# Performance work log

Measured on AMD Instinct MI355X. Metric: run time of the kernel, lower is better.

The kernel has to match this reference:

```python
import jax, jax.numpy as jnp
import numpy as np

D_MODEL = 512
NUM_HEADS = 8
LN_EPS = 1e-5


def _linear(x, W, b):
    # torch nn.Linear: y = x @ W.T + b, W is [out, in]
    return x @ W.T + b


def _layernorm(x, g, b):
    mu = jnp.mean(x, axis=-1, keepdims=True)
    var = jnp.mean((x - mu) ** 2, axis=-1, keepdims=True)
    return (x - mu) * jax.lax.rsqrt(var + LN_EPS) * g + b


def _proj_block(x, W1, b1, ln_g, ln_b, W2, b2):
    # Linear -> LayerNorm -> GELU(exact) -> Linear
    h = _linear(x, W1, b1)
    h = _layernorm(h, ln_g, ln_b)
    h = jax.nn.gelu(h, approximate=False)
    return _linear(h, W2, b2)


def setup_inputs() -> dict:
    key = jax.random.key(0)
    ks = jax.random.split(key, 16)
    d = D_MODEL
    B, N = 32, 50000
    s = 0.02
    inp = {
        "query_features": jax.random.normal(ks[0], (B, d), jnp.float32),
        "candidate_features": jax.random.normal(ks[1], (N, d), jnp.float32),
        # temperature param init: log(1/0.07)
        "temperature": jnp.asarray(np.log(1.0 / 0.07), jnp.float32),
        # query projection
        "qW1": jax.random.normal(ks[2], (d, d), jnp.float32) * s,
        "qb1": jnp.zeros((d,), jnp.float32),
        "q_ln_g": jnp.ones((d,), jnp.float32),
        "q_ln_b": jnp.zeros((d,), jnp.float32),
        "qW2": jax.random.normal(ks[3], (d, d), jnp.float32) * s,
        "qb2": jnp.zeros((d,), jnp.float32),
        # key projection
        "kW1": jax.random.normal(ks[4], (d, d), jnp.float32) * s,
        "kb1": jnp.zeros((d,), jnp.float32),
        "k_ln_g": jnp.ones((d,), jnp.float32),
        "k_ln_b": jnp.zeros((d,), jnp.float32),
        "kW2": jax.random.normal(ks[5], (d, d), jnp.float32) * s,
        "kb2": jnp.zeros((d,), jnp.float32),
        # MultiheadAttention in-proj (only q/k needed for attn weights)
        "in_proj_w": jax.random.normal(ks[6], (3 * d, d), jnp.float32) * s,
        "in_proj_b": jnp.zeros((3 * d,), jnp.float32),
        # similarity fusion MLP: 3 -> 64 -> 1
        "fW1": jax.random.normal(ks[7], (64, 3), jnp.float32) * 0.5,
        "fb1": jnp.zeros((64,), jnp.float32),
        "fW2": jax.random.normal(ks[8], (1, 64), jnp.float32) * 0.5,
        "fb2": jnp.zeros((1,), jnp.float32),
    }
    return inp


def reference(query_features, candidate_features, temperature,
              qW1, qb1, q_ln_g, q_ln_b, qW2, qb2,
              kW1, kb1, k_ln_g, k_ln_b, kW2, kb2,
              in_proj_w, in_proj_b, fW1, fb1, fW2, fb2):
    d = D_MODEL
    H = NUM_HEADS
    dh = d // H

    qp = _proj_block(query_features, qW1, qb1, q_ln_g, q_ln_b, qW2, qb2)      # [B, d]
    kp = _proj_block(candidate_features, kW1, kb1, k_ln_g, k_ln_b, kW2, kb2)  # [N, d]

    # 1) cosine similarity with learnable temperature
    qn = qp / jnp.linalg.norm(qp, axis=-1, keepdims=True)
    kn = kp / jnp.linalg.norm(kp, axis=-1, keepdims=True)
    cosine_sim = (qn @ kn.T) * jnp.exp(temperature)                            # [B, N]

    # 2) euclidean similarity (||q-k|| via quadratic expansion, no [B,N,D] temp)
    q2 = jnp.sum(qp * qp, axis=-1)[:, None]
    k2 = jnp.sum(kp * kp, axis=-1)[None, :]
    d2 = jnp.maximum(q2 + k2 - 2.0 * (qp @ kp.T), 0.0)
    euclidean_sim = 1.0 / (1.0 + jnp.sqrt(d2))                                 # [B, N]

    # 3) attention-weight similarity (torch MHA weights, averaged over heads)
    Wq, Wk = in_proj_w[:d], in_proj_w[d:2 * d]
    bq, bk = in_proj_b[:d], in_proj_b[d:2 * d]
    q = (_linear(qp, Wq, bq)).reshape(-1, H, dh)                               # [B, H, dh]
    k = (_linear(kp, Wk, bk)).reshape(-1, H, dh)                               # [N, H, dh]
    scores = jnp.einsum('bhd,nhd->bhn', q, k) / jnp.sqrt(jnp.float32(dh))      # [B, H, N]
    attn_w = jax.nn.softmax(scores, axis=-1)
    learned_sim = jnp.mean(attn_w, axis=1)                                     # [B, N]

    # fusion MLP over stacked [B, N, 3]
    sims = jnp.stack([cosine_sim, euclidean_sim, learned_sim], axis=-1)
    h = jax.nn.relu(_linear(sims, fW1, fb1))                                   # [B, N, 64]
    out = jax.nn.sigmoid(_linear(h, fW2, fb2))[..., 0]                         # [B, N]
    return out
```

## Files before the change

### kernel.cpp

```cpp
#include <hip/hip_runtime.h>
#include <math.h>

#define D    512
#define BQ   32
#define NH   8
#define MT   64
#define NT   512

typedef _Float16 h2  __attribute__((ext_vector_type(2)));
typedef _Float16 h4v __attribute__((ext_vector_type(4)));
typedef _Float16 h8  __attribute__((ext_vector_type(8)));
typedef float    f4  __attribute__((ext_vector_type(4)));

typedef const __attribute__((address_space(1))) void gas_void;
typedef __attribute__((address_space(3))) void las_void;

__device__ __forceinline__ f4 MF(h8 a, h8 b, f4 c) {
  return __builtin_amdgcn_mfma_f32_16x16x32_f16(a, b, c, 0, 0, 0);
}

__device__ __forceinline__ float erf_fast(float x) {
    float ax = fabsf(x);
    float tt = 1.0f / fmaf(0.3275911f, ax, 1.0f);
    float poly = tt * fmaf(tt, fmaf(tt, fmaf(tt, fmaf(tt, 1.061405429f, -1.453152027f),
                          1.421413741f), -0.284496736f), 0.254829592f);
    float r = 1.0f - poly * __expf(-ax * ax);
    return copysignf(r, x);
}
__device__ __forceinline__ float gelu_fast(float x) {
    return 0.5f * x * (1.0f + erf_fast(x * 0.7071067811865475f));
}
__device__ __forceinline__ float gelu_exact(float x) {
    return 0.5f * x * (1.0f + erff(x * 0.7071067811865475f));
}

__global__ __launch_bounds__(256) void qproj_kernel(
    const float* __restrict__ xq,
    const float* __restrict__ W1, const float* __restrict__ b1,
    const float* __restrict__ lng, const float* __restrict__ lnb,
    const float* __restrict__ W2, const float* __restrict__ b2,
    const float* __restrict__ Wio, const float* __restrict__ bio,
    float* __restrict__ qp, float* __restrict__ qv,
    float* __restrict__ q2o, float* __restrict__ qinvo,
    _Float16* __restrict__ qph)
{
    __shared__ float xs[D];
    __shared__ float hs[D];
    __shared__ float red[16];
    const int t = threadIdx.x;
    const int row = blockIdx.x;

    for (int i = t; i < D; i += 256) xs[i] = xq[row * D + i];
    __syncthreads();

    float a0 = 0.f, a1 = 0.f;
    for (int i = 0; i < D; i += 4) {
        float4 xv = *(const float4*)&xs[i];
        float4 w0 = *(const float4*)&W1[(size_t)t * D + i];
        float4 w1 = *(const float4*)&W1[(size_t)(t + 256) * D + i];
        a0 += xv.x*w0.x + xv.y*w0.y + xv.z*w0.z + xv.w*w0.w;
        a1 += xv.x*w1.x + xv.y*w1.y + xv.z*w1.z + xv.w*w1.w;
    }
    float h0 = a0 + b1[t], h1 = a1 + b1[t + 256];

    float s1 = h0 + h1, s2 = h0*h0 + h1*h1;
    for (int off = 32; off > 0; off >>= 1) { s1 += __shfl_down(s1, off); s2 += __shfl_down(s2, off); }
    if ((t & 63) == 0) { red[t >> 6] = s1; red[(t >> 6) + 4] = s2; }
    __syncthreads();
    if (t == 0) {
        float sa = red[0] + red[1] + red[2] + red[3];
        float sb = red[4] + red[5] + red[6] + red[7];
        float mu = sa / (float)D;
        red[8] = mu;
        red[9] = sb / (float)D - mu * mu;
    }
    __syncthreads();
    float mu = red[8];
    float isd = 1.0f / sqrtf(red[9] + 1e-5f);
    hs[t]       = gelu_exact((h0 - mu) * isd * lng[t]       + lnb[t]);
    hs[t + 256] = gelu_exact((h1 - mu) * isd * lng[t + 256] + lnb[t + 256]);
    __syncthreads();

    a0 = 0.f; a1 = 0.f;
    for (int i = 0; i < D; i += 4) {
        float4 gv = *(const float4*)&hs[i];
        float4 w0 = *(const float4*)&W2[(size_t)t * D + i];
        float4 w1 = *(const float4*)&W2[(size_t)(t + 256) * D + i];
        a0 += gv.x*w0.x + gv.y*w0.y + gv.z*w0.z + gv.w*w0.w;
        a1 += gv.x*w1.x + gv.y*w1.y + gv.z*w1.z + gv.w*w1.w;
    }
    float p0 = a0 + b2[t], p1 = a1 + b2[t + 256];
    qp[row * D + t] = p0;
    qp[row * D + t + 256] = p1;
    qph[row * D + t]       = (_Float16)(p0 * 32.0f);
    qph[row * D + t + 256] = (_Float16)(p1 * 32.0f);
    __syncthreads();
    xs[t] = p0; xs[t + 256] = p1;

    s1 = p0*p0 + p1*p1;
    for (int off = 32; off > 0; off >>= 1) s1 += __shfl_down(s1, off);
    if ((t & 63) == 0) red[t >> 6] = s1;
    __syncthreads();
    if (t == 0) {
        float sa = red[0] + red[1] + red[2] + red[3];
        q2o[row] = sa;
        qinvo[row] = 1.0f / sqrtf(sa);
    }
    __syncthreads();

    a0 = 0.f; a1 = 0.f;
    for (int i = 0; i < D; i += 4) {
        float4 pv = *(const float4*)&xs[i];
        float4 w0 = *(const float4*)&Wio[(size_t)t * D + i];
        float4 w1 = *(const float4*)&Wio[(size_t)(t + 256) * D + i];
        a0 += pv.x*w0.x + pv.y*w0.y + pv.z*w0.z + pv.w*w0.w;
        a1 += pv.x*w1.x + pv.y*w1.y + pv.z*w1.z + pv.w*w1.w;
    }
    qv[row * D + t]       = a0 + bio[t];
    qv[row * D + t + 256] = a1 + bio[t + 256];
}

__global__ __launch_bounds__(256) void wprep_kernel(
    const float* __restrict__ W1, const float* __restrict__ W2,
    _Float16* __restrict__ W1m, _Float16* __restrict__ W2m,
    float* __restrict__ sums)
{
    int idx = blockIdx.x * 256 + threadIdx.x;
    if (blockIdx.x == 0) sums[threadIdx.x] = 0.0f;
    if (idx >= D * D) return;
    W1m[idx] = (_Float16)(W1[idx] * 32.0f);
    W2m[idx] = (_Float16)(W2[idx] * 32.0f);
}

__global__ __launch_bounds__(256) void wtld_kernel(
    const float* __restrict__ qv, const float* __restrict__ Wio,
    _Float16* __restrict__ Wt)
{
    __shared__ float qs[64];
    const int bh = blockIdx.x, b = bh >> 3, h = bh & 7;
    const int t = threadIdx.x;
    if (t < 64) qs[t] = qv[b * D + h * 64 + t] * 0.125f;
    __syncthreads();
    const float* Wk = Wio + (size_t)D * D + (size_t)(h * 64) * D;
    float a0 = 0.f, a1 = 0.f;
    #pragma unroll 4
    for (int d = 0; d < 64; ++d) {
        float q = qs[d];
        a0 += q * Wk[(size_t)d * D + t];
        a1 += q * Wk[(size_t)d * D + t + 256];
    }
    Wt[(size_t)bh * D + t]       = (_Float16)a0;
    Wt[(size_t)bh * D + t + 256] = (_Float16)a1;
}

__global__ __launch_bounds__(NT) void cand_kernel(
    const float* __restrict__ xc, int N,
    const _Float16* __restrict__ W1m, const _Float16* __restrict__ W2m,
    const float* __restrict__ b1, const float* __restrict__ lng,
    const float* __restrict__ lnb, const float* __restrict__ b2,
    const _Float16* __restrict__ qph,
    const _Float16* __restrict__ Wt,
    const float* __restrict__ q2, const float* __restrict__ qinv,
    const float* __restrict__ tempp,
    float* __restrict__ cosw, float* __restrict__ eucw,
    _Float16* __restrict__ scw, float* __restrict__ sums)
{
    __shared__ _Float16 AH[MT * D];
    __shared__ __align__(16) unsigned char WBUF[65536];
    __shared__ __align__(16) float scr[MT * 33];
    __shared__ float k2p_[8 * MT];
    __shared__ float k2s_[MT], kins_[MT];
    __shared__ float lnmu_[MT], lnisd_[MT];

    float*  dotp_  = scr;
    float2* lnred_ = (float2*)scr;

    const int t    = threadIdx.x;
    const int wave = t >> 6;
    const int lane = t & 63;
    const int l16  = lane & 15;
    const int lK   = lane >> 4;
    const int wcol = wave * 64;
    const int n0   = blockIdx.x * MT;
    const int nvalid = min(MT, N - n0);
    const float expT = expf(tempp[0]);
    const float INVS = 1.0f / 1024.0f;
    const f4 fz = {0.f, 0.f, 0.f, 0.f};

    #pragma unroll
    for (int i = 0; i < 16; ++i) {
        int g = t + NT * i;
        int row = g >> 7;
        int c4 = (g & 127) * 4;
        f4 v = fz;
        if (n0 + row < N)
            v = __builtin_nontemporal_load((const f4*)(xc + (size_t)(n0 + row) * D + c4));
        h4v hi;
        #pragma unroll
        for (int e = 0; e < 4; ++e) hi[e] = (_Float16)(v[e] * 32.0f);
        *(h4v*)&AH[row * D + (c4 ^ ((row & 7) << 3))] = hi;
    }
    __syncthreads();

    const int sw = (l16 & 7) << 3;

    unsigned rdO[4];
    #pragma unroll
    for (int cb = 0; cb < 4; ++cb) {
        const int col = wcol + cb * 16 + l16;
        rdO[cb] = (unsigned)(col * 64 + ((lK ^ ((col >> 1) & 3)) << 4));
    }
    unsigned dstO[4];
    #pragma unroll
    for (int j = 0; j < 4; ++j) dstO[j] = (unsigned)(wave * 4096 + j * 1024);

    auto gemm = [&](const _Float16* __restrict__ Wm, f4 (&acc)[4][4]) {
        const _Float16* srcB[4];
        #pragma unroll
        for (int j = 0; j < 4; ++j) {
            const int col  = (wave * 4 + j) * 16 + (lane >> 2);
            const int slot = (lane & 3) ^ ((col >> 1) & 3);
            srcB[j] = Wm + (size_t)col * D + slot * 8;
        }
        auto stage = [&](int c, int buf) {
            #pragma unroll
            for (int j = 0; j < 4; ++j)
                __builtin_amdgcn_global_load_lds((gas_void*)(srcB[j] + c * 32),
                    (las_void*)(WBUF + buf * 32768 + dstO[j]), 16, 0, 0);
        };
        auto compute = [&](int c, int buf) {
            const unsigned char* wb = WBUF + buf * 32768;
            h8 bh[4];
            #pragma unroll
            for (int cb = 0; cb < 4; ++cb) bh[cb] = *(const h8*)(wb + rdO[cb]);
            const int ksw = (c * 32 + lK * 8) ^ sw;
            h8 ah[4];
            #pragma unroll
            for (int rb = 0; rb < 4; ++rb)
                ah[rb] = *(const h8*)&AH[(rb * 16 + l16) * D + ksw];
            #pragma unroll
            for (int rb = 0; rb < 4; ++rb)
                #pragma unroll
                for (int cb = 0; cb < 4; ++cb)
                    acc[rb][cb] = MF(ah[rb], bh[cb], acc[rb][cb]);
        };
        stage(0, 0); stage(1, 1);
        #pragma unroll 1
        for (int c = 0; c < 14; ++c) {
            const int buf = c & 1;
            asm volatile("s_waitcnt vmcnt(4)" ::: "memory");
            __builtin_amdgcn_sched_barrier(0);
            compute(c, buf);
            asm volatile("s_waitcnt lgkmcnt(0)" ::: "memory");
            __builtin_amdgcn_sched_barrier(0);
            stage(c + 2, buf);
            __builtin_amdgcn_sched_barrier(0);
        }
        asm volatile("s_waitcnt vmcnt(4)" ::: "memory");
        __builtin_amdgcn_sched_barrier(0);
        compute(14, 0);
        asm volatile("s_waitcnt vmcnt(0)" ::: "memory");
        __builtin_amdgcn_sched_barrier(0);
        compute(15, 1);
    };

    f4 acc[4][4];
    #pragma unroll
    for (int rb = 0; rb < 4; ++rb)
        #pragma unroll
        for (int cb = 0; cb < 4; ++cb) acc[rb][cb] = fz;

    gemm(W1m, acc);

    float s1a[4][4], s2a[4][4];
    #pragma unroll
    for (int rb = 0; rb < 4; ++rb)
        #pragma unroll
        for (int r = 0; r < 4; ++r) { s1a[rb][r] = 0.f; s2a[rb][r] = 0.f; }
    #pragma unroll
    for (int rb = 0; rb < 4; ++rb)
        #pragma unroll
        for (int cb = 0; cb < 4; ++cb) {
            const int j = wcol + cb * 16 + l16;
            const float bb = b1[j];
            #pragma unroll
            for (int r = 0; r < 4; ++r) {
                float v = acc[rb][cb][r] * INVS + bb;
                acc[rb][cb][r] = v;
                s1a[rb][r] += v;
                s2a[rb][r] += v * v;
            }
        }
    #pragma unroll
    for (int mm = 1; mm < 16; mm <<= 1)
        #pragma unroll
        for (int rb = 0; rb < 4; ++rb)
            #pragma unroll
            for (int r = 0; r < 4; ++r) {
                s1a[rb][r] += __shfl_xor(s1a[rb][r], mm);
                s2a[rb][r] += __shfl_xor(s2a[rb][r], mm);
            }
    if (l16 == 0) {
        #pragma unroll
        for (int rb = 0; rb < 4; ++rb)
            #pragma unroll
            for (int r = 0; r < 4; ++r)
                lnred_[wave * MT + rb * 16 + lK * 4 + r] = make_float2(s1a[rb][r], s2a[rb][r]);
    }
    __syncthreads();
    if (t < MT) {
        float sa = 0.f, sb = 0.f;
        #pragma unroll
        for (int w = 0; w < 8; ++w) { sa += lnred_[w * MT + t].x; sb += lnred_[w * MT + t].y; }
        float mu = sa * (1.0f / 512.0f);
        float var = sb * (1.0f / 512.0f) - mu * mu;
        lnmu_[t] = mu;
        lnisd_[t] = rsqrtf(var + 1e-5f);
    }
    __syncthreads();

    #pragma unroll
    for (int rb = 0; rb < 4; ++rb)
        #pragma unroll
        for (int cb = 0; cb < 4; ++cb) {
            const int j = wcol + cb * 16 + l16;
            const float gg = lng[j], bb = lnb[j];
            #pragma unroll
            for (int r = 0; r < 4; ++r) {
                const int m = rb * 16 + lK * 4 + r;
                float v = (acc[rb][cb][r] - lnmu_[m]) * lnisd_[m] * gg + bb;
                v = gelu_fast(v) * 32.0f;
                AH[m * D + (j ^ ((m & 7) << 3))] = (_Float16)v;
            }
        }
    __syncthreads();

    #pragma unroll
    for (int rb = 0; rb < 4; ++rb)
        #pragma unroll
        for (int cb = 0; cb < 4; ++cb) acc[rb][cb] = fz;
    gemm(W2m, acc);

    float ss[4][4];
    #pragma unroll
    for (int rb = 0; rb < 4; ++rb)
        #pragma unroll
        for (int r = 0; r < 4; ++r) ss[rb][r] = 0.f;
    #pragma unroll
    for (int rb = 0; rb < 4; ++rb)
        #pragma unroll
        for (int cb = 0; cb < 4; ++cb) {
            const int j = wcol + cb * 16 + l16;
            const float bb = b2[j];
            #pragma unroll
            for (int r = 0; r < 4; ++r) {
                float v = acc[rb][cb][r] * INVS + bb;
                acc[rb][cb][r] = v;
                ss[rb][r] += v * v;
            }
        }
    #pragma unroll
    for (int mm = 1; mm < 16; mm <<= 1)
        #pragma unroll
        for (int rb = 0; rb < 4; ++rb)
            #pragma unroll
            for (int r = 0; r < 4; ++r)
                ss[rb][r] += __shfl_xor(ss[rb][r], mm);
    __syncthreads();
    if (l16 == 0) {
        #pragma unroll
        for (int rb = 0; rb < 4; ++rb)
            #pragma unroll
            for (int r = 0; r < 4; ++r)
                k2p_[wave * MT + rb * 16 + lK * 4 + r] = ss[rb][r];
    }
    #pragma unroll
    for (int rb = 0; rb < 4; ++rb)
        #pragma unroll
        for (int cb = 0; cb < 4; ++cb) {
            const int j = wcol + cb * 16 + l16;
            #pragma unroll
            for (int r = 0; r < 4; ++r) {
                const int m = rb * 16 + lK * 4 + r;
                AH[m * D + (j ^ ((m & 7) << 3))] = (_Float16)(acc[rb][cb][r] * 32.0f);
            }
        }
    __syncthreads();

    if (t < MT) {
        float sa = 0.f;
        #pragma unroll
        for (int w = 0; w < 8; ++w) sa += k2p_[w * MT + t];
        k2s_[t] = sa;
        kins_[t] = rsqrtf(fmaxf(sa, 1e-30f));
    }

    f4 as[4][2];
    #pragma unroll
    for (int rb = 0; rb < 4; ++rb) { as[rb][0] = fz; as[rb][1] = fz; }
    {
        const _Float16* wsrcB[2];
        #pragma unroll
        for (int j = 0; j < 2; ++j) {
            const int rr   = j * 16 + (lane >> 2);
            const int slot = (lane & 3) ^ ((rr >> 1) & 3);
            wsrcB[j] = Wt + (size_t)(wave * 32 + rr) * D + slot * 8;
        }
        auto stageWT = [&](int c, int buf) {
            #pragma unroll
            for (int j = 0; j < 2; ++j)
                __builtin_amdgcn_global_load_lds((gas_void*)(wsrcB[j] + c * 32),
                    (las_void*)(WBUF + buf * 16384 + wave * 2048 + j * 1024), 16, 0, 0);
        };
        const unsigned wrd0 = (unsigned)(l16 * 64 + ((lK ^ ((l16 >> 1) & 3)) << 4));
        auto scoreChunk = [&](int c, int buf) {
            const unsigned char* wb = WBUF + buf * 16384 + wave * 2048;
            h8 w0 = *(const h8*)(wb + wrd0);
            h8 w1 = *(const h8*)(wb + 1024 + wrd0);
            const int ksw = (c * 32 + lK * 8) ^ sw;
            #pragma unroll
            for (int rb = 0; rb < 4; ++rb) {
                h8 a = *(const h8*)&AH[(rb * 16 + l16) * D + ksw];
                as[rb][0] = MF(a, w0, as[rb][0]);
                as[rb][1] = MF(a, w1, as[rb][1]);
            }
        };
        stageWT(0, 0); stageWT(1, 1); stageWT(2, 2);
        #pragma unroll 4
        for (int c = 0; c < 12; ++c) {
            asm volatile("s_waitcnt vmcnt(4)" ::: "memory");
            __builtin_amdgcn_sched_barrier(0);
            scoreChunk(c, c & 3);
            asm volatile("s_waitcnt lgkmcnt(0)" ::: "memory");
            __builtin_amdgcn_sched_barrier(0);
            stageWT(c + 3, (c + 3) & 3);
            __builtin_amdgcn_sched_barrier(0);
        }
        asm volatile("s_waitcnt vmcnt(4)" ::: "memory");
        __builtin_amdgcn_sched_barrier(0);
        scoreChunk(12, 0);
        asm volatile("s_waitcnt lgkmcnt(0)" ::: "memory");
        __builtin_amdgcn_sched_barrier(0);
        stageWT(15, 3);
        __builtin_amdgcn_sched_barrier(0);
        asm volatile("s_waitcnt vmcnt(4)" ::: "memory");
        __builtin_amdgcn_sched_barrier(0);
        scoreChunk(13, 1);
        asm volatile("s_waitcnt vmcnt(2)" ::: "memory");
        __builtin_amdgcn_sched_barrier(0);
        scoreChunk(14, 2);
        asm volatile("s_waitcnt vmcnt(0)" ::: "memory");
        __builtin_amdgcn_sched_barrier(0);
        scoreChunk(15, 3);
    }

    {
        float part[2] = {0.f, 0.f};
        #pragma unroll
        for (int cb = 0; cb < 2; ++cb)
            #pragma unroll
            for (int rb = 0; rb < 4; ++rb)
                #pragma unroll
                for (int r = 0; r < 4; ++r) {
                    const int n = rb * 16 + lK * 4 + r;
                    if (n < nvalid)
                        part[cb] += __expf(as[rb][cb][r] * (1.0f / 32.0f));
                }
        #pragma unroll
        for (int cb = 0; cb < 2; ++cb) {
            part[cb] += __shfl_xor(part[cb], 16);
            part[cb] += __shfl_xor(part[cb], 32);
        }
        if (lK == 0) {
            atomicAdd(&sums[wave * 32 + l16], part[0]);
            atomicAdd(&sums[wave * 32 + 16 + l16], part[1]);
        }
    }

    {
        const int rq = wave >> 1, cbq = wave & 1;
        f4 ad = fz;
        const int ra = (rq * 16 + l16) * D;
        const int j = cbq * 16 + l16;
        #pragma unroll 2
        for (int ks = 0; ks < 16; ++ks) {
            const int k0 = ks * 32 + lK * 8;
            const int ksw = k0 ^ sw;
            h8 ah0 = *(const h8*)&AH[ra + ksw];
            h8 bh = *(const h8*)&qph[j * D + k0];
            ad = MF(ah0, bh, ad);
        }
        #pragma unroll
        for (int r = 0; r < 4; ++r)
            dotp_[(rq * 16 + lK * 4 + r) * 33 + cbq * 16 + l16] = ad[r];
    }
    __syncthreads();

    for (int p = t; p < BQ * MT; p += NT) {
        const int m = p & (MT - 1), b = p >> 6;
        if (m < nvalid) {
            float dt = dotp_[m * 33 + b] * INVS;
            __builtin_nontemporal_store(dt * qinv[b] * kins_[m] * expT,
                                        &cosw[(size_t)b * N + n0 + m]);
            float dd = q2[b] + k2s_[m] - 2.0f * dt;
            __builtin_nontemporal_store(1.0f / (1.0f + sqrtf(fmaxf(dd, 0.f))),
                                        &eucw[(size_t)b * N + n0 + m]);
        }
    }

    _Float16* SC = AH;
    {
        const int bh0 = wave * 32 + l16;
        #pragma unroll
        for (int cb = 0; cb < 2; ++cb) {
            const int bhc = bh0 + cb * 16;
            const int b = bhc >> 3, h = bhc & 7;
            #pragma unroll
            for (int rb = 0; rb < 4; ++rb) {
                #pragma unroll
                for (int r = 0; r < 4; ++r) {
                    const int n = rb * 16 + lK * 4 + r;
                    SC[n * 256 + ((b ^ (n & 31)) * 8) + h] =
                        (_Float16)(as[rb][cb][r] * (1.0f / 32.0f));
                }
            }
        }
    }
    __syncthreads();

    #pragma unroll
    for (int p = t; p < BQ * MT; p += NT) {
        const int b = p >> 6, n = p & (MT - 1);
        if (n < nvalid) {
            h8 v = *(const h8*)&SC[n * 256 + ((b ^ (n & 31)) * 8)];
            __builtin_nontemporal_store(v, (h8*)&scw[((size_t)b * N + n0 + n) * NH]);
        }
    }
}

__global__ __launch_bounds__(256) void final_kernel(
    const float* __restrict__ cosw, const float* __restrict__ eucw,
    const _Float16* __restrict__ scw, int N,
    const float* __restrict__ sums,
    const float* __restrict__ fW1, const float* __restrict__ fb1,
    const float* __restrict__ fW2, const float* __restrict__ fb2,
    float* __restrict__ out, int total)
{
    __shared__ float w1s[192], b1s[64], w2s[64];
    __shared__ float sis[BQ * NH];
    __shared__ float b2s;
    const int t = threadIdx.x;
    if (t < 192) w1s[t] = fW1[t];
    else { b1s[t - 192] = fb1[t - 192]; w2s[t - 192] = fW2[t - 192]; }
    sis[t] = 1.0f / sums[t];
    if (t == 0) b2s = fb2[0];
    __syncthreads();

    const int idx = blockIdx.x * 256 + t;
    if (idx >= total) return;
    const int b = idx / N;

    float c = cosw[idx], e = eucw[idx];
    h8 v = *(const h8*)&scw[(size_t)idx * NH];
    float ls = 0.f;
    #pragma unroll
    for (int h = 0; h < NH; ++h)
        ls += __expf((float)v[h]) * sis[b * NH + h];
    ls *= 0.125f;

    float logit = b2s;
    #pragma unroll
    for (int j = 0; j < 64; ++j) {
        float hj = fmaf(w1s[j*3], c, fmaf(w1s[j*3+1], e, fmaf(w1s[j*3+2], ls, b1s[j])));
        logit = fmaf(w2s[j], fmaxf(hj, 0.f), logit);
    }
    out[idx] = 1.0f / (1.0f + expf(-logit));
}

extern "C" void kernel_launch(void* const* d_in, const int* in_sizes, int n_in,
                              void* d_out, int out_size, void* d_ws, size_t ws_size,
                              hipStream_t stream)
{
    const float* xq   = (const float*)d_in[0];
    const float* xc   = (const float*)d_in[1];
    const float* temp = (const float*)d_in[2];
    const float* qW1  = (const float*)d_in[3];
    const float* qb1  = (const float*)d_in[4];
    const float* qlg  = (const float*)d_in[5];
    const float* qlb  = (const float*)d_in[6];
    const float* qW2  = (const float*)d_in[7];
    const float* qb2  = (const float*)d_in[8];
    const float* kW1  = (const float*)d_in[9];
    const float* kb1  = (const float*)d_in[10];
    const float* klg  = (const float*)d_in[11];
    const float* klb  = (const float*)d_in[12];
    const float* kW2  = (const float*)d_in[13];
    const float* kb2  = (const float*)d_in[14];
    const float* Wio  = (const float*)d_in[15];
    const float* bio  = (const float*)d_in[16];
    const float* fW1  = (const float*)d_in[17];
    const float* fb1  = (const float*)d_in[18];
    const float* fW2  = (const float*)d_in[19];
    const float* fb2  = (const float*)d_in[20];

    const int N = in_sizes[1] / D;

    float* ws   = (float*)d_ws;
    float* qp   = ws;
    float* qv   = qp + BQ * D;
    float* q2   = qv + BQ * D;
    float* qinv = q2 + BQ;
    float* sinv = qinv + BQ;
    float* sums = sinv + BQ * NH;
    float* cosw = sums + BQ * NH;
    float* eucw = cosw + (size_t)BQ * N;
    float* fend = eucw + (size_t)BQ * N;

    _Float16* hb  = (_Float16*)fend;
    _Float16* W1m = hb;
    _Float16* W2m = W1m + D * D;
    _Float16* qph = W2m + D * D;
    _Float16* Wt  = qph + BQ * D;
    _Float16* scw = Wt + BQ * NH * D;

    qproj_kernel<<<BQ, 256, 0, stream>>>(xq, qW1, qb1, qlg, qlb, qW2, qb2,
                                         Wio, bio, qp, qv, q2, qinv, qph);

    wprep_kernel<<<(D * D + 255) / 256, 256, 0, stream>>>(kW1, kW2, W1m, W2m, sums);

    wtld_kernel<<<BQ * NH, 256, 0, stream>>>(qv, Wio, Wt);

    const int nblk = (N + MT - 1) / MT;
    cand_kernel<<<nblk, NT, 0, stream>>>(xc, N, W1m, W2m,
                                         kb1, klg, klb, kb2,
                                         qph, Wt, q2, qinv, temp,
                                         cosw, eucw, scw, sums);

    const int total = BQ * N;
    final_kernel<<<(total + 255) / 256, 256, 0, stream>>>(cosw, eucw, scw, N, sums,
                                                          fW1, fb1, fW2, fb2,
                                                          (float*)d_out, total);
}
```

Measured before the change: 339.2 us.

## Drop fp16 scaling, move exp into cand kernel, split q in-proj into wtld

Removes the x32 fp16 pre-scaling of weights, activations and query features along with the matching 1/1024 rescales in the candidate kernel. Exponentials of attention scores are now computed once in the candidate kernel and stored as fp16, so the final kernel only multiplies. The query projection kernel now runs with 512 threads at one output per thread, and the per-head query in-projection moves into the wtld kernel. Dropping the scaling risks fp16 underflow or loss of precision, and storing exp values in fp16 risks overflow.

```diff
diff --git a/kernel.cpp b/kernel.cpp
--- a/kernel.cpp
+++ b/kernel.cpp
@@ -34,90 +34,71 @@
     return 0.5f * x * (1.0f + erff(x * 0.7071067811865475f));
 }
 
-__global__ __launch_bounds__(256) void qproj_kernel(
+__global__ __launch_bounds__(512) void qproj_kernel(
     const float* __restrict__ xq,
     const float* __restrict__ W1, const float* __restrict__ b1,
     const float* __restrict__ lng, const float* __restrict__ lnb,
     const float* __restrict__ W2, const float* __restrict__ b2,
-    const float* __restrict__ Wio, const float* __restrict__ bio,
-    float* __restrict__ qp, float* __restrict__ qv,
+    float* __restrict__ qp,
     float* __restrict__ q2o, float* __restrict__ qinvo,
     _Float16* __restrict__ qph)
 {
     __shared__ float xs[D];
     __shared__ float hs[D];
-    __shared__ float red[16];
+    __shared__ float red[20];
     const int t = threadIdx.x;
     const int row = blockIdx.x;
-
-    for (int i = t; i < D; i += 256) xs[i] = xq[row * D + i];
-    __syncthreads();
-
-    float a0 = 0.f, a1 = 0.f;
+    const int wave = t >> 6, lane = t & 63;
+
+    xs[t] = xq[row * D + t];
+    __syncthreads();
+
+    float a0 = 0.f;
     for (int i = 0; i < D; i += 4) {
         float4 xv = *(const float4*)&xs[i];
         float4 w0 = *(const float4*)&W1[(size_t)t * D + i];
-        float4 w1 = *(const float4*)&W1[(size_t)(t + 256) * D + i];
         a0 += xv.x*w0.x + xv.y*w0.y + xv.z*w0.z + xv.w*w0.w;
-        a1 += xv.x*w1.x + xv.y*w1.y + xv.z*w1.z + xv.w*w1.w;
-    }
-    float h0 = a0 + b1[t], h1 = a1 + b1[t + 256];
-
-    float s1 = h0 + h1, s2 = h0*h0 + h1*h1;
+    }
+    float h0 = a0 + b1[t];
+
+    float s1 = h0, s2 = h0 * h0;
     for (int off = 32; off > 0; off >>= 1) { s1 += __shfl_down(s1, off); s2 += __shfl_down(s2, off); }
-    if ((t & 63) == 0) { red[t >> 6] = s1; red[(t >> 6) + 4] = s2; }
+    if (lane == 0) { red[wave] = s1; red[8 + wave] = s2; }
     __syncthreads();
     if (t == 0) {
-        float sa = red[0] + red[1] + red[2] + red[3];
-        float sb = red[4] + red[5] + red[6] + red[7];
+        float sa = 0.f, sb = 0.f;
+        #pragma unroll
+        for (int w = 0; w < 8; ++w) { sa += red[w]; sb += red[8 + w]; }
         float mu = sa / (float)D;
-        red[8] = mu;
-        red[9] = sb / (float)D - mu * mu;
-    }
-    __syncthreads();
-    float mu = red[8];
-    float isd = 1.0f / sqrtf(red[9] + 1e-5f);
-    hs[t]       = gelu_exact((h0 - mu) * isd * lng[t]       + lnb[t]);
-    hs[t + 256] = gelu_exact((h1 - mu) * isd * lng[t + 256] + lnb[t + 256]);
-    __syncthreads();
-
-    a0 = 0.f; a1 = 0.f;
+        red[16] = mu;
+        red[17] = rsqrtf(sb / (float)D - mu * mu + 1e-5f);
+    }
+    __syncthreads();
+    float mu = red[16], isd = red[17];
+    hs[t] = gelu_exact((h0 - mu) * isd * lng[t] + lnb[t]);
+    __syncthreads();
+
+    a0 = 0.f;
     for (int i = 0; i < D; i += 4) {
         float4 gv = *(const float4*)&hs[i];
         float4 w0 = *(const float4*)&W2[(size_t)t * D + i];
-        float4 w1 = *(const float4*)&W2[(size_t)(t + 256) * D + i];
         a0 += gv.x*w0.x + gv.y*w0.y + gv.z*w0.z + gv.w*w0.w;
-        a1 += gv.x*w1.x + gv.y*w1.y + gv.z*w1.z + gv.w*w1.w;
-    }
-    float p0 = a0 + b2[t], p1 = a1 + b2[t + 256];
-    qp[row * D + t] = p0;
-    qp[row * D + t + 256] = p1;
-    qph[row * D + t]       = (_Float16)(p0 * 32.0f);
-    qph[row * D + t + 256] = (_Float16)(p1 * 32.0f);
-    __syncthreads();
-    xs[t] = p0; xs[t + 256] = p1;
-
-    s1 = p0*p0 + p1*p1;
+    }
+    float p0 = a0 + b2[t];
+    qp[row * D + t]  = p0;
+    qph[row * D + t] = (_Float16)p0;
+
+    s1 = p0 * p0;
     for (int off = 32; off > 0; off >>= 1) s1 += __shfl_down(s1, off);
-    if ((t & 63) == 0) red[t >> 6] = s1;
+    if (lane == 0) red[wave] = s1;
     __syncthreads();
     if (t == 0) {
-        float sa = red[0] + red[1] + red[2] + red[3];
+        float sa = 0.f;
+        #pragma unroll
+        for (int w = 0; w < 8; ++w) sa += red[w];
         q2o[row] = sa;
         qinvo[row] = 1.0f / sqrtf(sa);
     }
-    __syncthreads();
-
-    a0 = 0.f; a1 = 0.f;
-    for (int i = 0; i < D; i += 4) {
-        float4 pv = *(const float4*)&xs[i];
-        float4 w0 = *(const float4*)&Wio[(size_t)t * D + i];
-        float4 w1 = *(const float4*)&Wio[(size_t)(t + 256) * D + i];
-        a0 += pv.x*w0.x + pv.y*w0.y + pv.z*w0.z + pv.w*w0.w;
-        a1 += pv.x*w1.x + pv.y*w1.y + pv.z*w1.z + pv.w*w1.w;
-    }
-    qv[row * D + t]       = a0 + bio[t];
-    qv[row * D + t + 256] = a1 + bio[t + 256];
 }
 
 __global__ __launch_bounds__(256) void wprep_kernel(
@@ -128,19 +109,41 @@
     int idx = blockIdx.x * 256 + threadIdx.x;
     if (blockIdx.x == 0) sums[threadIdx.x] = 0.0f;
     if (idx >= D * D) return;
-    W1m[idx] = (_Float16)(W1[idx] * 32.0f);
-    W2m[idx] = (_Float16)(W2[idx] * 32.0f);
+    W1m[idx] = (_Float16)W1[idx];
+    W2m[idx] = (_Float16)W2[idx];
 }
 
 __global__ __launch_bounds__(256) void wtld_kernel(
-    const float* __restrict__ qv, const float* __restrict__ Wio,
+    const float* __restrict__ qp, const float* __restrict__ Wio,
+    const float* __restrict__ bio,
     _Float16* __restrict__ Wt)
 {
+    __shared__ float qpb[D];
     __shared__ float qs[64];
     const int bh = blockIdx.x, b = bh >> 3, h = bh & 7;
     const int t = threadIdx.x;
-    if (t < 64) qs[t] = qv[b * D + h * 64 + t] * 0.125f;
-    __syncthreads();
+
+    qpb[t]       = qp[b * D + t];
+    qpb[t + 256] = qp[b * D + t + 256];
+    __syncthreads();
+
+    {
+        const int d = t >> 2, part = t & 3;
+        const float* Wq = Wio + (size_t)(h * 64 + d) * D + part * 128;
+        const float* xp = qpb + part * 128;
+        float a = 0.f;
+        #pragma unroll 8
+        for (int i = 0; i < 128; i += 4) {
+            float4 xv = *(const float4*)&xp[i];
+            float4 wv = *(const float4*)&Wq[i];
+            a += xv.x*wv.x + xv.y*wv.y + xv.z*wv.z + xv.w*wv.w;
+        }
+        a += __shfl_xor(a, 1);
+        a += __shfl_xor(a, 2);
+        if (part == 0) qs[d] = (a + bio[h * 64 + d]) * 0.125f;
+    }
+    __syncthreads();
+
     const float* Wk = Wio + (size_t)D * D + (size_t)(h * 64) * D;
     float a0 = 0.f, a1 = 0.f;
     #pragma unroll 4
@@ -184,7 +187,6 @@
     const int n0   = blockIdx.x * MT;
     const int nvalid = min(MT, N - n0);
     const float expT = expf(tempp[0]);
-    const float INVS = 1.0f / 1024.0f;
     const f4 fz = {0.f, 0.f, 0.f, 0.f};
 
     #pragma unroll
@@ -197,7 +199,7 @@
             v = __builtin_nontemporal_load((const f4*)(xc + (size_t)(n0 + row) * D + c4));
         h4v hi;
         #pragma unroll
-        for (int e = 0; e < 4; ++e) hi[e] = (_Float16)(v[e] * 32.0f);
+        for (int e = 0; e < 4; ++e) hi[e] = (_Float16)v[e];
         *(h4v*)&AH[row * D + (c4 ^ ((row & 7) << 3))] = hi;
     }
     __syncthreads();
@@ -285,7 +287,7 @@
             const float bb = b1[j];
             #pragma unroll
             for (int r = 0; r < 4; ++r) {
-                float v = acc[rb][cb][r] * INVS + bb;
+                float v = acc[rb][cb][r] + bb;
                 acc[rb][cb][r] = v;
                 s1a[rb][r] += v;
                 s2a[rb][r] += v * v;
@@ -329,8 +331,7 @@
             for (int r = 0; r < 4; ++r) {
                 const int m = rb * 16 + lK * 4 + r;
                 float v = (acc[rb][cb][r] - lnmu_[m]) * lnisd_[m] * gg + bb;
-                v = gelu_fast(v) * 32.0f;
-                AH[m * D + (j ^ ((m & 7) << 3))] = (_Float16)v;
+                AH[m * D + (j ^ ((m & 7) << 3))] = (_Float16)gelu_fast(v);
             }
         }
     __syncthreads();
@@ -354,7 +355,7 @@
             const float bb = b2[j];
             #pragma unroll
             for (int r = 0; r < 4; ++r) {
-                float v = acc[rb][cb][r] * INVS + bb;
+                float v = acc[rb][cb][r] + bb;
                 acc[rb][cb][r] = v;
                 ss[rb][r] += v * v;
             }
@@ -382,7 +383,7 @@
             #pragma unroll
             for (int r = 0; r < 4; ++r) {
                 const int m = rb * 16 + lK * 4 + r;
-                AH[m * D + (j ^ ((m & 7) << 3))] = (_Float16)(acc[rb][cb][r] * 32.0f);
+                AH[m * D + (j ^ ((m & 7) << 3))] = (_Float16)acc[rb][cb][r];
             }
         }
     __syncthreads();
@@ -455,6 +456,13 @@
     }
 
     {
+        #pragma unroll
+        for (int cb = 0; cb < 2; ++cb)
+            #pragma unroll
+            for (int rb = 0; rb < 4; ++rb)
+                #pragma unroll
+                for (int r = 0; r < 4; ++r)
+                    as[rb][cb][r] = __expf(as[rb][cb][r]);
         float part[2] = {0.f, 0.f};
         #pragma unroll
         for (int cb = 0; cb < 2; ++cb)
@@ -463,8 +471,7 @@
                 #pragma unroll
                 for (int r = 0; r < 4; ++r) {
                     const int n = rb * 16 + lK * 4 + r;
-                    if (n < nvalid)
-                        part[cb] += __expf(as[rb][cb][r] * (1.0f / 32.0f));
+                    if (n < nvalid) part[cb] += as[rb][cb][r];
                 }
         #pragma unroll
         for (int cb = 0; cb < 2; ++cb) {
@@ -499,7 +506,7 @@
     for (int p = t; p < BQ * MT; p += NT) {
         const int m = p & (MT - 1), b = p >> 6;
         if (m < nvalid) {
-            float dt = dotp_[m * 33 + b] * INVS;
+            float dt = dotp_[m * 33 + b];
             __builtin_nontemporal_store(dt * qinv[b] * kins_[m] * expT,
                                         &cosw[(size_t)b * N + n0 + m]);
             float dd = q2[b] + k2s_[m] - 2.0f * dt;
@@ -520,8 +527,7 @@
                 #pragma unroll
                 for (int r = 0; r < 4; ++r) {
                     const int n = rb * 16 + lK * 4 + r;
-                    SC[n * 256 + ((b ^ (n & 31)) * 8) + h] =
-                        (_Float16)(as[rb][cb][r] * (1.0f / 32.0f));
+                    SC[n * 256 + ((b ^ (n & 31)) * 8) + h] = (_Float16)as[rb][cb][r];
                 }
             }
         }
@@ -552,7 +558,7 @@
     const int t = threadIdx.x;
     if (t < 192) w1s[t] = fW1[t];
     else { b1s[t - 192] = fb1[t - 192]; w2s[t - 192] = fW2[t - 192]; }
-    sis[t] = 1.0f / sums[t];
+    sis[t] = 0.125f / sums[t];
     if (t == 0) b2s = fb2[0];
     __syncthreads();
 
@@ -565,8 +571,7 @@
     float ls = 0.f;
     #pragma unroll
     for (int h = 0; h < NH; ++h)
-        ls += __expf((float)v[h]) * sis[b * NH + h];
-    ls *= 0.125f;
+        ls += (float)v[h] * sis[b * NH + h];
 
     float logit = b2s;
     #pragma unroll
@@ -623,12 +628,12 @@
     _Float16* Wt  = qph + BQ * D;
     _Float16* scw = Wt + BQ * NH * D;
 
-    qproj_kernel<<<BQ, 256, 0, stream>>>(xq, qW1, qb1, qlg, qlb, qW2, qb2,
-                                         Wio, bio, qp, qv, q2, qinv, qph);
-
     wprep_kernel<<<(D * D + 255) / 256, 256, 0, stream>>>(kW1, kW2, W1m, W2m, sums);
 
-    wtld_kernel<<<BQ * NH, 256, 0, stream>>>(qv, Wio, Wt);
+    qproj_kernel<<<BQ, 512, 0, stream>>>(xq, qW1, qb1, qlg, qlb, qW2, qb2,
+                                         qp, q2, qinv, qph);
+
+    wtld_kernel<<<BQ * NH, 256, 0, stream>>>(qp, Wio, bio, Wt);
 
     const int nblk = (N + MT - 1) / MT;
     cand_kernel<<<nblk, NT, 0, stream>>>(xc, N, W1m, W2m,
```

After: 311.5 us. 1.09x faster.
